# Optimization experiments

Measured on AMD Instinct MI355X. Metric: run time of the kernel, lower is better.

The kernel has to match this reference:

```python
import jax, jax.numpy as jnp
import numpy as np

# db4 decomposition low-pass filter (pywt convention, 8 taps)
DEC_LO = np.array([-0.010597401784997278, 0.032883011666982945, 0.030841381835986965,
                   -0.18703481171888114, -0.02798376941698385, 0.6308807679295904,
                   0.7148465705525415, 0.23037781330885523], dtype=np.float32)
L = DEC_LO.shape[0]  # 8
REC_LO = DEC_LO[::-1].copy()
DEC_HI = (REC_LO * ((-1.0) ** (np.arange(L) + 1))).astype(np.float32)
REC_HI = DEC_HI[::-1].copy()
LEVEL = 7

# lax.conv does correlation; flip filters to get true convolution (pywt semantics)
K_DEC = jnp.asarray(np.stack([DEC_LO[::-1], DEC_HI[::-1]])[:, None, :])  # [2,1,L] out-ch: (lo, hi)
K_REC = jnp.asarray(np.stack([REC_LO[::-1], REC_HI[::-1]])[None, :, :])  # [1,2,L] in-ch: (ca, cd)


def dwt(x):
    # x: [B, N]. pywt zero-mode dwt == full conv then take odd indices;
    # fused here as stride-2 conv with asymmetric padding (L-2, L-1).
    y = jax.lax.conv_general_dilated(x[:, None, :], K_DEC, (2,), [(L - 2, L - 1)])
    return y[:, 0], y[:, 1]  # each [B, floor((N+L-1)/2)]


def idwt(ca, cd):
    # upsample-by-2 (lhs_dilation, length 2n-1), full conv, trim L-2 each side -> pad (1,1)
    y = jax.lax.conv_general_dilated(jnp.stack([ca, cd], axis=1), K_REC, (1,),
                                     [(1, 1)], lhs_dilation=(2,))
    return y[:, 0]  # [B, 2n - L + 2]


def soft(c, t):
    # pywt.threshold(mode='soft')
    return jnp.sign(c) * jnp.maximum(jnp.abs(c) - t, 0.0)


def setup_inputs() -> dict:
    key = jax.random.key(0)
    k1, k2 = jax.random.split(key)
    x = jax.random.normal(k1, (32768, 1116), dtype=jnp.float32)
    # learned scalar parameter, initialized like nn.Parameter(torch.tensor(0.02))
    raw_threshold = jnp.asarray(0.02, dtype=jnp.float32)
    return {"x": x, "raw_threshold": raw_threshold}


def reference(x, raw_threshold):
    thr = jnp.maximum(raw_threshold, 0.01)  # torch.clamp(min=0.01)
    # wavedec: 7-level analysis
    a = x
    details = []
    for _ in range(LEVEL):
        a, d = dwt(a)
        details.append(d)
    # soft-threshold every coefficient band (including approximation)
    a = soft(a, thr)
    details = [soft(d, thr) for d in details]
    # waverec: synthesis, truncating cA when one sample longer than cD (pywt rule)
    for d in reversed(details):
        if a.shape[-1] > d.shape[-1]:
            a = a[:, : d.shape[-1]]
        a = idwt(a, d)
    return a  # [B, 1116]
```

## Files before the change

### kernel.cpp

```cpp
#include <hip/hip_runtime.h>

#define NT 256
#define NCOL 1116
#define NLEV 7

typedef float v2f __attribute__((ext_vector_type(2)));

static constexpr float DEC_LO[8] = {-0.010597401784997278f,  0.032883011666982945f,
                                     0.030841381835986965f, -0.18703481171888114f,
                                    -0.02798376941698385f,   0.6308807679295904f,
                                     0.7148465705525415f,    0.23037781330885523f};
static constexpr float DEC_HI[8] = {-0.23037781330885523f,   0.7148465705525415f,
                                    -0.6308807679295904f,   -0.02798376941698385f,
                                     0.18703481171888114f,   0.030841381835986965f,
                                    -0.032883011666982945f, -0.010597401784997278f};
static constexpr float REC_LO[8] = { 0.23037781330885523f,   0.7148465705525415f,
                                     0.6308807679295904f,   -0.02798376941698385f,
                                    -0.18703481171888114f,   0.030841381835986965f,
                                     0.032883011666982945f, -0.010597401784997278f};
static constexpr float REC_HI[8] = {-0.010597401784997278f, -0.032883011666982945f,
                                     0.030841381835986965f,  0.18703481171888114f,
                                    -0.02798376941698385f,  -0.6308807679295904f,
                                     0.7148465705525415f,   -0.23037781330885523f};

static constexpr int ALEN[8] = {1116, 561, 284, 145, 76, 41, 24, 15};
static constexpr int DOFF[7] = {0, 562, 846, 992, 1068, 1110, 1136};

static __device__ __forceinline__ float softf(float c, float t) {
    float m = fabsf(c) - t;
    return m > 0.0f ? copysignf(m, c) : 0.0f;
}

static __device__ __forceinline__ v2f vfma(float c, v2f v, v2f a) {
#if __has_builtin(__builtin_elementwise_fma)
    return __builtin_elementwise_fma((v2f){c, c}, v, a);
#else
    v2f r; r.x = fmaf(c, v.x, a.x); r.y = fmaf(c, v.y, a.y); return r;
#endif
}

template <int L, bool LAST>
static __device__ __forceinline__ void fwd_level(const float* cur, float* nxt, float* dp,
                                                 float thr, int tid) {
    constexpr int nout = ALEN[L + 1];
    constexpr int ntask = (nout + 1) / 2;
    for (int t = tid; t < ntask; t += NT) {
        const float* src = cur + 4 * t - 6;
        float4 w0 = *(const float4*)src;
        float4 w1 = *(const float4*)(src + 4);
        float4 w2 = *(const float4*)(src + 8);
        float w[12] = {w0.x, w0.y, w0.z, w0.w, w1.x, w1.y, w1.z, w1.w,
                       w2.x, w2.y, w2.z, w2.w};
        v2f lo = {0.f, 0.f}, hi = {0.f, 0.f};
#pragma unroll
        for (int s = 0; s < 8; ++s) {
            v2f v = {w[7 - s], w[9 - s]};
            lo = vfma(DEC_LO[s], v, lo);
            hi = vfma(DEC_HI[s], v, hi);
        }
        if (LAST) { lo.x = softf(lo.x, thr); lo.y = softf(lo.y, thr); }
        hi.x = softf(hi.x, thr);
        hi.y = softf(hi.y, thr);
        *(v2f*)(dp + 2 * t) = hi;
        if (!(nout & 1) || (2 * t + 1 < nout)) {
            *(v2f*)(nxt + 2 * t) = lo;
        } else {
            nxt[2 * t] = lo.x;
        }
    }
    if (!LAST) {
        if (tid < 6) nxt[-6 + tid] = 0.0f;
        if (tid < 10) nxt[nout + tid] = 0.0f;
    }
}

template <int L, bool FINAL>
static __device__ __forceinline__ void inv_level(const float* ca, const float* dp,
                                                 float* y, int tid) {
    constexpr int M = ALEN[L + 1];
    constexpr int npair = M - 3;
    constexpr int ntask = (npair + 1) / 2;
    for (int t = tid; t < ntask; t += NT) {
        const float* cap = ca + 2 * t;
        const float* ddp = dp + 2 * t;
        float2 a01 = *(const float2*)cap;
        float2 a23 = *(const float2*)(cap + 2);
        float  a4  = cap[4];
        float2 d01 = *(const float2*)ddp;
        float2 d23 = *(const float2*)(ddp + 2);
        float  d4  = ddp[4];
        float aw[5] = {a01.x, a01.y, a23.x, a23.y, a4};
        float dw[5] = {d01.x, d01.y, d23.x, d23.y, d4};
        v2f ye = {0.f, 0.f}, yo = {0.f, 0.f};
#pragma unroll
        for (int k = 0; k < 4; ++k) {
            v2f va = {aw[3 - k], aw[4 - k]};
            v2f vd = {dw[3 - k], dw[4 - k]};
            ye = vfma(REC_LO[2 * k],     va, ye);
            yo = vfma(REC_LO[2 * k + 1], va, yo);
            ye = vfma(REC_HI[2 * k],     vd, ye);
            yo = vfma(REC_HI[2 * k + 1], vd, yo);
        }
        if (FINAL) {
            *(float4*)(y + 4 * t) = make_float4(ye.x, yo.x, ye.y, yo.y);
        } else {
            *(v2f*)(y + 4 * t)     = (v2f){ye.x, yo.x};
            *(v2f*)(y + 4 * t + 2) = (v2f){ye.y, yo.y};
        }
    }
}

__global__ __launch_bounds__(NT)
void wavelet_kernel(const float* __restrict__ x,
                    const float* __restrict__ thr_ptr,
                    float* __restrict__ out) {
    __shared__ __align__(16) float A[1136];
    __shared__ __align__(16) float B[580];
    __shared__ __align__(16) float D[1154];

    const int tid = threadIdx.x;
    const float thr = fmaxf(thr_ptr[0], 0.01f);
    float* a0 = A + 6;
    float* b0 = B + 6;

    {
        const float4* xr = (const float4*)(x + (size_t)blockIdx.x * NCOL);
        for (int i = tid; i < NCOL / 4; i += NT) {
            float4 v = xr[i];
            *(v2f*)(a0 + 4 * i)     = (v2f){v.x, v.y};
            *(v2f*)(a0 + 4 * i + 2) = (v2f){v.z, v.w};
        }
        if (tid < 6)  A[tid] = 0.0f;
        if (tid < 10) a0[NCOL + tid] = 0.0f;
    }
    __syncthreads();

    fwd_level<0, false>(a0, b0, D + DOFF[0], thr, tid); __syncthreads();
    fwd_level<1, false>(b0, a0, D + DOFF[1], thr, tid); __syncthreads();
    fwd_level<2, false>(a0, b0, D + DOFF[2], thr, tid); __syncthreads();
    fwd_level<3, false>(b0, a0, D + DOFF[3], thr, tid); __syncthreads();
    fwd_level<4, false>(a0, b0, D + DOFF[4], thr, tid); __syncthreads();
    fwd_level<5, false>(b0, a0, D + DOFF[5], thr, tid); __syncthreads();
    fwd_level<6, true >(a0, b0, D + DOFF[6], thr, tid); __syncthreads();

    inv_level<6, false>(b0, D + DOFF[6], a0, tid); __syncthreads();
    inv_level<5, false>(a0, D + DOFF[5], b0, tid); __syncthreads();
    inv_level<4, false>(b0, D + DOFF[4], a0, tid); __syncthreads();
    inv_level<3, false>(a0, D + DOFF[3], b0, tid); __syncthreads();
    inv_level<2, false>(b0, D + DOFF[2], a0, tid); __syncthreads();
    inv_level<1, false>(a0, D + DOFF[1], b0, tid); __syncthreads();

    float* orow = out + (size_t)blockIdx.x * NCOL;
    inv_level<0, true>(b0, D + DOFF[0], orow, tid);
}

extern "C" void kernel_launch(void* const* d_in, const int* in_sizes, int n_in,
                              void* d_out, int out_size, void* d_ws, size_t ws_size,
                              hipStream_t stream) {
    const float* x = (const float*)d_in[0];
    const float* thr = (const float*)d_in[1];
    float* out = (float*)d_out;
    const int nrow = in_sizes[0] / NCOL;
    hipLaunchKernelGGL(wavelet_kernel, dim3(nrow), dim3(NT), 0, stream, x, thr, out);
}
```

Baseline: 277.6 us.

## Shrink block to 64 threads and compute four outputs per thread per level

The block size drops from 256 to a single 64-thread wavefront, and each thread in the forward and inverse levels now produces four coefficients instead of two, using wider vector loads and stores. Shared-memory offsets and padding are adjusted so the wider tasks can write zero tails and the left padding of B is zeroed once up front. The aim is to cut idle threads in the small coarse levels and raise per-thread ILP, with more blocks resident per CU. The cost is fewer threads per row, so the large first levels need multiple loop iterations per thread, plus higher register pressure.

Measured after the change: 294.3 us. 6.0% more time.

```diff
diff --git a/kernel.cpp b/kernel.cpp
--- a/kernel.cpp
+++ b/kernel.cpp
@@ -1,6 +1,6 @@
 #include <hip/hip_runtime.h>
 
-#define NT 256
+#define NT 64
 #define NCOL 1116
 #define NLEV 7
 
@@ -24,7 +24,7 @@
                                      0.7148465705525415f,   -0.23037781330885523f};
 
 static constexpr int ALEN[8] = {1116, 561, 284, 145, 76, 41, 24, 15};
-static constexpr int DOFF[7] = {0, 562, 846, 992, 1068, 1110, 1136};
+static constexpr int DOFF[7] = {0, 564, 848, 996, 1072, 1116, 1140};
 
 static __device__ __forceinline__ float softf(float c, float t) {
     float m = fabsf(c) - t;
@@ -43,35 +43,35 @@
 static __device__ __forceinline__ void fwd_level(const float* cur, float* nxt, float* dp,
                                                  float thr, int tid) {
     constexpr int nout = ALEN[L + 1];
-    constexpr int ntask = (nout + 1) / 2;
+    constexpr int ntask = (nout + 3) / 4;
     for (int t = tid; t < ntask; t += NT) {
-        const float* src = cur + 4 * t - 6;
+        const float* src = cur + 8 * t - 6;
         float4 w0 = *(const float4*)src;
         float4 w1 = *(const float4*)(src + 4);
         float4 w2 = *(const float4*)(src + 8);
-        float w[12] = {w0.x, w0.y, w0.z, w0.w, w1.x, w1.y, w1.z, w1.w,
-                       w2.x, w2.y, w2.z, w2.w};
-        v2f lo = {0.f, 0.f}, hi = {0.f, 0.f};
+        float4 w3 = *(const float4*)(src + 12);
+        float w[16] = {w0.x, w0.y, w0.z, w0.w, w1.x, w1.y, w1.z, w1.w,
+                       w2.x, w2.y, w2.z, w2.w, w3.x, w3.y, w3.z, w3.w};
+        v2f loA = {0.f, 0.f}, loB = {0.f, 0.f}, hiA = {0.f, 0.f}, hiB = {0.f, 0.f};
 #pragma unroll
         for (int s = 0; s < 8; ++s) {
-            v2f v = {w[7 - s], w[9 - s]};
-            lo = vfma(DEC_LO[s], v, lo);
-            hi = vfma(DEC_HI[s], v, hi);
+            v2f vA = {w[7 - s],  w[9 - s]};
+            v2f vB = {w[11 - s], w[13 - s]};
+            loA = vfma(DEC_LO[s], vA, loA);
+            hiA = vfma(DEC_HI[s], vA, hiA);
+            loB = vfma(DEC_LO[s], vB, loB);
+            hiB = vfma(DEC_HI[s], vB, hiB);
         }
-        if (LAST) { lo.x = softf(lo.x, thr); lo.y = softf(lo.y, thr); }
-        hi.x = softf(hi.x, thr);
-        hi.y = softf(hi.y, thr);
-        *(v2f*)(dp + 2 * t) = hi;
-        if (!(nout & 1) || (2 * t + 1 < nout)) {
-            *(v2f*)(nxt + 2 * t) = lo;
-        } else {
-            nxt[2 * t] = lo.x;
+        if (LAST) {
+            loA.x = softf(loA.x, thr); loA.y = softf(loA.y, thr);
+            loB.x = softf(loB.x, thr); loB.y = softf(loB.y, thr);
         }
+        *(float4*)(dp + 4 * t) = make_float4(softf(hiA.x, thr), softf(hiA.y, thr),
+                                             softf(hiB.x, thr), softf(hiB.y, thr));
+        *(v2f*)(nxt + 4 * t)     = loA;
+        *(v2f*)(nxt + 4 * t + 2) = loB;
     }
-    if (!LAST) {
-        if (tid < 6) nxt[-6 + tid] = 0.0f;
-        if (tid < 10) nxt[nout + tid] = 0.0f;
-    }
+    if (tid < 14) nxt[4 * ntask + tid] = 0.0f;
 }
 
 template <int L, bool FINAL>
@@ -79,33 +79,42 @@
                                                  float* y, int tid) {
     constexpr int M = ALEN[L + 1];
     constexpr int npair = M - 3;
-    constexpr int ntask = (npair + 1) / 2;
+    constexpr int ntask = (npair + 3) / 4;
     for (int t = tid; t < ntask; t += NT) {
-        const float* cap = ca + 2 * t;
-        const float* ddp = dp + 2 * t;
+        const float* cap = ca + 4 * t;
         float2 a01 = *(const float2*)cap;
         float2 a23 = *(const float2*)(cap + 2);
-        float  a4  = cap[4];
-        float2 d01 = *(const float2*)ddp;
-        float2 d23 = *(const float2*)(ddp + 2);
-        float  d4  = ddp[4];
-        float aw[5] = {a01.x, a01.y, a23.x, a23.y, a4};
-        float dw[5] = {d01.x, d01.y, d23.x, d23.y, d4};
-        v2f ye = {0.f, 0.f}, yo = {0.f, 0.f};
+        float2 a45 = *(const float2*)(cap + 4);
+        float2 a67 = *(const float2*)(cap + 6);
+        float4 dq0 = *(const float4*)(dp + 4 * t);
+        float4 dq1 = *(const float4*)(dp + 4 * t + 4);
+        float aw[8] = {a01.x, a01.y, a23.x, a23.y, a45.x, a45.y, a67.x, a67.y};
+        float dw[8] = {dq0.x, dq0.y, dq0.z, dq0.w, dq1.x, dq1.y, dq1.z, dq1.w};
+        v2f yeA = {0.f, 0.f}, yoA = {0.f, 0.f}, yeB = {0.f, 0.f}, yoB = {0.f, 0.f};
 #pragma unroll
         for (int k = 0; k < 4; ++k) {
-            v2f va = {aw[3 - k], aw[4 - k]};
-            v2f vd = {dw[3 - k], dw[4 - k]};
-            ye = vfma(REC_LO[2 * k],     va, ye);
-            yo = vfma(REC_LO[2 * k + 1], va, yo);
-            ye = vfma(REC_HI[2 * k],     vd, ye);
-            yo = vfma(REC_HI[2 * k + 1], vd, yo);
+            v2f vaA = {aw[3 - k], aw[4 - k]};
+            v2f vdA = {dw[3 - k], dw[4 - k]};
+            v2f vaB = {aw[5 - k], aw[6 - k]};
+            v2f vdB = {dw[5 - k], dw[6 - k]};
+            yeA = vfma(REC_LO[2 * k],     vaA, yeA);
+            yoA = vfma(REC_LO[2 * k + 1], vaA, yoA);
+            yeA = vfma(REC_HI[2 * k],     vdA, yeA);
+            yoA = vfma(REC_HI[2 * k + 1], vdA, yoA);
+            yeB = vfma(REC_LO[2 * k],     vaB, yeB);
+            yoB = vfma(REC_LO[2 * k + 1], vaB, yoB);
+            yeB = vfma(REC_HI[2 * k],     vdB, yeB);
+            yoB = vfma(REC_HI[2 * k + 1], vdB, yoB);
         }
         if (FINAL) {
-            *(float4*)(y + 4 * t) = make_float4(ye.x, yo.x, ye.y, yo.y);
+            *(float4*)(y + 8 * t) = make_float4(yeA.x, yoA.x, yeA.y, yoA.y);
+            if (4 * t + 2 < npair)
+                *(float4*)(y + 8 * t + 4) = make_float4(yeB.x, yoB.x, yeB.y, yoB.y);
         } else {
-            *(v2f*)(y + 4 * t)     = (v2f){ye.x, yo.x};
-            *(v2f*)(y + 4 * t + 2) = (v2f){ye.y, yo.y};
+            *(v2f*)(y + 8 * t)     = (v2f){yeA.x, yoA.x};
+            *(v2f*)(y + 8 * t + 2) = (v2f){yeA.y, yoA.y};
+            *(v2f*)(y + 8 * t + 4) = (v2f){yeB.x, yoB.x};
+            *(v2f*)(y + 8 * t + 6) = (v2f){yeB.y, yoB.y};
         }
     }
 }
@@ -114,9 +123,9 @@
 void wavelet_kernel(const float* __restrict__ x,
                     const float* __restrict__ thr_ptr,
                     float* __restrict__ out) {
-    __shared__ __align__(16) float A[1136];
-    __shared__ __align__(16) float B[580];
-    __shared__ __align__(16) float D[1154];
+    __shared__ __align__(16) float A[1140];
+    __shared__ __align__(16) float B[588];
+    __shared__ __align__(16) float D[1156];
 
     const int tid = threadIdx.x;
     const float thr = fmaxf(thr_ptr[0], 0.01f);
@@ -130,8 +139,8 @@
             *(v2f*)(a0 + 4 * i)     = (v2f){v.x, v.y};
             *(v2f*)(a0 + 4 * i + 2) = (v2f){v.z, v.w};
         }
-        if (tid < 6)  A[tid] = 0.0f;
-        if (tid < 10) a0[NCOL + tid] = 0.0f;
+        if (tid < 6)  { A[tid] = 0.0f; B[tid] = 0.0f; }
+        if (tid < 14) a0[NCOL + tid] = 0.0f;
     }
     __syncthreads();
 
```
